# Optimization experiments

Measured on AMD Instinct MI355X. Metric: run time of the kernel, lower is better.

## Reference

```python
import jax, jax.numpy as jnp
import numpy as np

S, HID, H, KH, D = 2048, 3584, 28, 4, 128
G = H // KH  # GQA group size = 7
EPS = 1e-6
THETA = 1000000.0


def _rmsnorm(x, w, eps=EPS):
    v = jnp.mean(x.astype(jnp.float32) ** 2, axis=-1, keepdims=True)
    return (x * jax.lax.rsqrt(v + eps)).astype(x.dtype) * w


def setup_inputs() -> dict:
    key = jax.random.key(0)
    k1, k2, k3, k4 = jax.random.split(key, 4)
    return {
        "positions": jnp.arange(S, dtype=jnp.int32),
        "hidden_states": jax.random.normal(k1, (S, HID), dtype=jnp.float32),
        "qkv_w": jax.random.normal(k2, ((H + 2 * KH) * D, HID), dtype=jnp.float32) * (1.0 / np.sqrt(HID)),
        "qkv_b": jax.random.normal(k3, ((H + 2 * KH) * D,), dtype=jnp.float32) * 0.02,
        "q_norm_w": jnp.ones((H * D,), dtype=jnp.float32),
        "k_norm_w": jnp.ones((KH * D,), dtype=jnp.float32),
        "o_w": jax.random.normal(k4, (HID, H * D), dtype=jnp.float32) * (1.0 / np.sqrt(H * D)),
    }


def reference(positions, hidden_states, qkv_w, qkv_b, q_norm_w, k_norm_w, o_w):
    # QKV projection (fused linear, bias=True)
    qkv = hidden_states @ qkv_w.T + qkv_b  # [S, (H+2*KH)*D]
    q, k, v = jnp.split(qkv, [H * D, H * D + KH * D], axis=-1)

    # olmo-style QK RMSNorm over the full (all-heads-concatenated) q/k vectors
    q = _rmsnorm(q, q_norm_w)
    k = _rmsnorm(k, k_norm_w)

    # NeoX-style RoPE (vLLM default): rotate halves
    half = D // 2
    inv_freq = 1.0 / (THETA ** (jnp.arange(0, D, 2, dtype=jnp.float32) / D))  # [D/2]
    freqs = positions[:, None].astype(jnp.float32) * inv_freq  # [S, D/2]
    cos = jnp.cos(freqs)[:, None, :]  # [S, 1, D/2]
    sin = jnp.sin(freqs)[:, None, :]

    def rope(x, nh):
        x = x.reshape(S, nh, D)
        x1, x2 = x[..., :half], x[..., half:]
        return jnp.concatenate([x1 * cos - x2 * sin, x2 * cos + x1 * sin], axis=-1)

    q = rope(q, H)            # [S, H, D]
    k = rope(k, KH)           # [S, KH, D]
    v = v.reshape(S, KH, D)   # [S, KH, D]

    # Grouped-query causal attention
    qg = q.reshape(S, KH, G, D)
    scores = jnp.einsum('skgd,tkd->kgst', qg, k) * (D ** -0.5)  # [KH, G, S, S]
    causal = positions[:, None] >= positions[None, :]  # [S, S]
    scores = jnp.where(causal[None, None], scores, jnp.finfo(scores.dtype).min)
    probs = jax.nn.softmax(scores, axis=-1)
    attn = jnp.einsum('kgst,tkd->skgd', probs, v).reshape(S, H * D)

    # Output projection (bias=False)
    return attn @ o_w.T  # [S, HID]
```

## Files before the change

### kernel.cpp

```cpp
#include <hip/hip_runtime.h>
#include <hip/hip_bf16.h>
#include <stdint.h>

#define S_LEN 2048
#define HIDDEN 3584
#define NH 28
#define NKH 4
#define DH 128
#define NG 7
#define NQKV 4608
#define QD 3584
#define KD 512

using bf16x8 = __attribute__((ext_vector_type(8))) __bf16;
using f32x4  = __attribute__((ext_vector_type(4))) float;
using f32x16 = __attribute__((ext_vector_type(16))) float;

#define AS3(p) ((__attribute__((address_space(3))) void*)(p))
#define AS1(p) ((const __attribute__((address_space(1))) void*)(p))

__device__ __forceinline__ unsigned short f2bf(float f) {
    unsigned u = __float_as_uint(f);
    u += 0x7FFFu + ((u >> 16) & 1u);
    return (unsigned short)(u >> 16);
}
__device__ __forceinline__ unsigned cvtpk(float a, float b) {
    unsigned r;
    asm("v_cvt_pk_bf16_f32 %0, %1, %2" : "=v"(r) : "v"(a), "v"(b));
    return r;
}

__global__ void cvt2_f32_bf16(const float* __restrict__ a, unsigned short* __restrict__ oa, int na4,
                              const float* __restrict__ b, unsigned short* __restrict__ ob, int nb4) {
    int i = blockIdx.x * blockDim.x + threadIdx.x;
    const float* src;
    unsigned short* dst;
    int n;
    if (i < na4)            { src = a; dst = oa; n = i; }
    else if (i < na4 + nb4) { src = b; dst = ob; n = i - na4; }
    else return;
    float4 v = ((const float4*)src)[n];
    ushort4 o;
    o.x = f2bf(v.x); o.y = f2bf(v.y); o.z = f2bf(v.z); o.w = f2bf(v.w);
    ((ushort4*)dst)[n] = o;
}

__global__ void cvt_f32_bf16(const float* __restrict__ in,
                             unsigned short* __restrict__ out, int n4) {
    int i = blockIdx.x * blockDim.x + threadIdx.x;
    if (i >= n4) return;
    float4 v = ((const float4*)in)[i];
    ushort4 o;
    o.x = f2bf(v.x); o.y = f2bf(v.y); o.z = f2bf(v.z); o.w = f2bf(v.w);
    ((ushort4*)out)[i] = o;
}

template<int BN>
__global__ __launch_bounds__(512, 2) void gemm_deep(
    const unsigned short* __restrict__ A,
    const unsigned short* __restrict__ B,
    float* __restrict__ C,
    const float* __restrict__ bias,
    int M, int N, int K)
{
    constexpr int NF    = BN / 64;
    constexpr int WN    = BN / 4;
    constexpr int VB    = BN / 64;
    constexpr int TILEB = (256 + BN) * 128;
    __shared__ __align__(16) unsigned char ds[2 * TILEB];

    const int tid  = threadIdx.x;
    const int w    = tid >> 6;
    const int lane = tid & 63;
    const int lr   = lane & 15;
    const int lg   = lane >> 4;
    const int wr   = w >> 2;
    const int wc   = w & 3;
    const int m0   = blockIdx.y * 256;
    const int n0   = blockIdx.x * BN;
    const long K2  = (long)K * 2;
    const int scw  = 16 * ((tid & 7) ^ ((tid >> 3) & 7));
    const int srow = tid >> 3;
    const unsigned char* Ab = (const unsigned char*)A;
    const unsigned char* Bb = (const unsigned char*)B;
    const int nk = K >> 6;

    unsigned char* buf0 = ds;
    unsigned char* buf1 = ds + TILEB;

    auto stageB = [&](int kt, unsigned char* bufp) {
        const long kb = (long)kt * 128;
        #pragma unroll
        for (int k = 0; k < VB; ++k)
            __builtin_amdgcn_global_load_lds(
                AS1(Bb + (long)(n0 + k * 64 + srow) * K2 + kb + scw),
                AS3(bufp + k * 8192 + w * 1024), 16, 0, 0);
    };
    auto stageA = [&](int kt, unsigned char* bufp) {
        const long kb = (long)kt * 128;
        #pragma unroll
        for (int k = 0; k < 4; ++k)
            __builtin_amdgcn_global_load_lds(
                AS1(Ab + (long)(m0 + k * 64 + srow) * K2 + kb + scw),
                AS3(bufp + VB * 8192 + k * 8192 + w * 1024), 16, 0, 0);
    };

    f32x4  acc[8][NF] = {};
    bf16x8 af[4][2], bf[NF][2];

    auto readA = [&](const unsigned char* bufp, int half) {
        #pragma unroll
        for (int i = 0; i < 4; ++i) {
            const int row = wr * 128 + (half * 4 + i) * 16 + lr;
            #pragma unroll
            for (int kk = 0; kk < 2; ++kk)
                af[i][kk] = *(const bf16x8*)(bufp + VB * 8192 + row * 128 +
                                             ((kk * 64 + lg * 16) ^ ((lr & 7) << 4)));
        }
    };
    auto readB = [&](const unsigned char* bufp) {
        #pragma unroll
        for (int ni = 0; ni < NF; ++ni) {
            const int row = wc * WN + ni * 16 + lr;
            #pragma unroll
            for (int kk = 0; kk < 2; ++kk)
                bf[ni][kk] = *(const bf16x8*)(bufp + row * 128 +
                                              ((kk * 64 + lg * 16) ^ ((lr & 7) << 4)));
        }
    };
    auto mfmah = [&](int half) {
        __builtin_amdgcn_s_setprio(1);
        #pragma unroll
        for (int i = 0; i < 4; ++i)
            #pragma unroll
            for (int ni = 0; ni < NF; ++ni)
                #pragma unroll
                for (int kk = 0; kk < 2; ++kk)
                    acc[half * 4 + i][ni] = __builtin_amdgcn_mfma_f32_16x16x32_bf16(
                        af[i][kk], bf[ni][kk], acc[half * 4 + i][ni], 0, 0, 0);
        __builtin_amdgcn_s_setprio(0);
    };

    #define VMC() do { if constexpr (VB == 3) asm volatile("s_waitcnt vmcnt(3)" ::: "memory"); \
                       else                   asm volatile("s_waitcnt vmcnt(2)" ::: "memory"); } while (0)
    #define LGK0() do { asm volatile("s_waitcnt lgkmcnt(0)" ::: "memory"); \
                        __builtin_amdgcn_sched_barrier(0); } while (0)

    stageB(0, buf0); stageA(0, buf0); stageB(1, buf1);
    VMC();
    __builtin_amdgcn_s_barrier();

    const int npairs = nk >> 1;
    for (int p = 0; p < npairs; ++p) {
        const int to = 2 * p + 1;
        int te2 = 2 * p + 2; if (te2 >= nk) te2 = nk - 1;
        int to2 = 2 * p + 3; if (to2 >= nk) to2 = nk - 1;

        readA(buf0, 0); readB(buf0);
        stageA(to, buf1);
        __builtin_amdgcn_s_barrier();
        LGK0();
        mfmah(0);
        __builtin_amdgcn_s_barrier();
        readA(buf0, 1);
        stageB(te2, buf0);
        __builtin_amdgcn_s_barrier();
        LGK0();
        mfmah(1);
        VMC();
        __builtin_amdgcn_s_barrier();
        readA(buf1, 0); readB(buf1);
        stageA(te2, buf0);
        __builtin_amdgcn_s_barrier();
        LGK0();
        mfmah(0);
        __builtin_amdgcn_s_barrier();
        readA(buf1, 1);
        stageB(to2, buf1);
        __builtin_amdgcn_s_barrier();
        LGK0();
        mfmah(1);
        VMC();
        __builtin_amdgcn_s_barrier();
    }
    asm volatile("s_waitcnt vmcnt(0)" ::: "memory");

    #pragma unroll
    for (int mi = 0; mi < 8; ++mi) {
        #pragma unroll
        for (int ni = 0; ni < NF; ++ni) {
            const int col = n0 + wc * WN + ni * 16 + lr;
            const float bv = bias ? bias[col] : 0.0f;
            #pragma unroll
            for (int j = 0; j < 4; ++j) {
                const int row = m0 + wr * 128 + mi * 16 + lg * 4 + j;
                C[(long)row * N + col] = acc[mi][ni][j] + bv;
            }
        }
    }
    #undef VMC
    #undef LGK0
}

__global__ __launch_bounds__(256) void qkv_post(
    const float* __restrict__ qkv,
    const int* __restrict__ positions,
    const float* __restrict__ qnw,
    const float* __restrict__ knw,
    unsigned short* __restrict__ qb,
    unsigned short* __restrict__ kb,
    unsigned short* __restrict__ vt2)
{
    const int s   = blockIdx.x;
    const int tid = threadIdx.x;
    const float* rowp = qkv + (long)s * NQKV;
    __shared__ float red[256];
    __shared__ float s_rq, s_rk;

    float aq = 0.f;
    for (int i = tid; i < QD; i += 256) { float v = rowp[i]; aq += v * v; }
    red[tid] = aq; __syncthreads();
    for (int off = 128; off > 0; off >>= 1) {
        if (tid < off) red[tid] += red[tid + off];
        __syncthreads();
    }
    if (tid == 0) s_rq = rsqrtf(red[0] / (float)QD + 1e-6f);
    __syncthreads();

    float ak = 0.f;
    for (int i = tid; i < KD; i += 256) { float v = rowp[QD + i]; ak += v * v; }
    red[tid] = ak; __syncthreads();
    for (int off = 128; off > 0; off >>= 1) {
        if (tid < off) red[tid] += red[tid + off];
        __syncthreads();
    }
    if (tid == 0) s_rk = rsqrtf(red[0] / (float)KD + 1e-6f);
    __syncthreads();

    const float rq  = s_rq, rk = s_rk * 0.08838834764831845f;
    const float pos = (float)positions[s];
    const float c_lnf = 0.21586735253866598f;

    for (int u = tid; u < NH * 64; u += 256) {
        const int h = u >> 6, j = u & 63;
        const float inv = expf(-(float)j * c_lnf);
        float sn, cs;
        sincosf(pos * inv, &sn, &cs);
        const float x1 = rowp[h * DH + j]      * rq * qnw[h * DH + j];
        const float x2 = rowp[h * DH + 64 + j] * rq * qnw[h * DH + 64 + j];
        qb[((long)h * S_LEN + s) * DH + j]      = f2bf(x1 * cs - x2 * sn);
        qb[((long)h * S_LEN + s) * DH + 64 + j] = f2bf(x2 * cs + x1 * sn);
    }
    for (int u = tid; u < NKH * 64; u += 256) {
        const int h = u >> 6, j = u & 63;
        const float inv = expf(-(float)j * c_lnf);
        float sn, cs;
        sincosf(pos * inv, &sn, &cs);
        const float x1 = rowp[QD + h * DH + j]      * rk * knw[h * DH + j];
        const float x2 = rowp[QD + h * DH + 64 + j] * rk * knw[h * DH + 64 + j];
        kb[((long)h * S_LEN + s) * DH + j]      = f2bf(x1 * cs - x2 * sn);
        kb[((long)h * S_LEN + s) * DH + 64 + j] = f2bf(x2 * cs + x1 * sn);
    }
    for (int u = tid; u < KD; u += 256) {
        const int hh = u >> 7, d = u & 127;
        vt2[(((long)hh * (S_LEN / 32) + (s >> 5)) * DH + d) * 32 + (s & 31)] =
            f2bf(rowp[QD + KD + u]);
    }
}

__global__ __launch_bounds__(512) void attn_fwd(
    const unsigned short* __restrict__ qb,
    const unsigned short* __restrict__ kb,
    const unsigned short* __restrict__ vt2,
    unsigned short* __restrict__ attnb)
{
    __shared__ __align__(16) unsigned char sK[2][8192];
    __shared__ __align__(16) unsigned char sV[2][8192];

    const int qt   = 63 - blockIdx.x;
    const int kh   = blockIdx.y;
    const int tid  = threadIdx.x;
    const int w    = tid >> 6;
    const int lane = tid & 63;
    const int lq   = lane & 31;
    const int hi   = lane >> 5;
    const int hi8  = hi * 8;
    const int hi4  = hi * 4;
    const int q0   = qt * 32;
    const int NT   = qt + 1;

    const unsigned char* kgb = (const unsigned char*)(kb + (long)kh * S_LEN * DH);
    const unsigned char* vgb = (const unsigned char*)vt2 + (long)kh * (S_LEN / 32) * 8192;

    const int ksrc_off = (((tid & 15) ^ (tid >> 4)) & 15) << 4;
    const int u        = tid & 255;
    const int vsrc_off = ((u & 3) ^ ((u >> 3) & 3)) << 4;

    const float RTHR = 8.0f;

    bf16x8 qf[8];
    if (w < 7) {
        const int h = kh * NG + w;
        const unsigned short* qrow = qb + ((long)h * S_LEN + q0 + lq) * DH;
        #pragma unroll
        for (int c = 0; c < 8; ++c)
            qf[c] = *(const bf16x8*)(qrow + c * 16 + hi8);
    }

    f32x16 o[4] = {};
    float m = -3e38f;
    float l = 0.f;

    if (tid < 256) {
        #pragma unroll
        for (int j = 0; j < 2; ++j)
            __builtin_amdgcn_global_load_lds(AS1(kgb + ((tid >> 4) + 16 * j) * 256 + ksrc_off),
                                             AS3(&sK[0][0] + w * 1024 + j * 4096), 16, 0, 0);
    } else {
        #pragma unroll
        for (int j = 0; j < 2; ++j)
            __builtin_amdgcn_global_load_lds(AS1(vgb + ((u >> 2) + 64 * j) * 64 + vsrc_off),
                                             AS3(&sV[0][0] + (w - 4) * 1024 + j * 4096), 16, 0, 0);
    }

    for (int t = 0; t < NT; ++t) {
        __syncthreads();

        if (t + 1 < NT) {
            const int b = (t + 1) & 1;
            if (tid < 256) {
                const unsigned char* ks = kgb + (long)(t + 1) * 8192;
                #pragma unroll
                for (int j = 0; j < 2; ++j)
                    __builtin_amdgcn_global_load_lds(AS1(ks + ((tid >> 4) + 16 * j) * 256 + ksrc_off),
                                                     AS3(&sK[b][0] + w * 1024 + j * 4096), 16, 0, 0);
            } else {
                const unsigned char* vs = vgb + (long)(t + 1) * 8192;
                #pragma unroll
                for (int j = 0; j < 2; ++j)
                    __builtin_amdgcn_global_load_lds(AS1(vs + ((u >> 2) + 64 * j) * 64 + vsrc_off),
                                                     AS3(&sV[b][0] + (w - 4) * 1024 + j * 4096), 16, 0, 0);
            }
        }

        if (w < 7) {
            const unsigned char* sKb = sK[t & 1];
            const unsigned char* sVb = sV[t & 1];

            bf16x8 kf[8];
            #pragma unroll
            for (int c = 0; c < 8; ++c)
                kf[c] = *(const bf16x8*)(sKb + lq * 256 + (((2 * c + hi) ^ (lq & 15)) << 4));
            f32x16 sc = {};
            #pragma unroll
            for (int c = 0; c < 8; ++c)
                sc = __builtin_amdgcn_mfma_f32_32x32x16_bf16(kf[c], qf[c], sc, 0, 0, 0);

            float s[16];
            if (t == NT - 1) {
                #pragma unroll
                for (int r = 0; r < 16; ++r) {
                    const int kr = (r & 3) + 8 * (r >> 2) + hi4;
                    s[r] = (kr > lq) ? -3e38f : sc[r];
                }
            } else {
                #pragma unroll
                for (int r = 0; r < 16; ++r) s[r] = sc[r];
            }

            float mx = s[0];
            #pragma unroll
            for (int r = 1; r < 16; ++r) mx = fmaxf(mx, s[r]);
            mx = fmaxf(mx, __shfl_xor(mx, 32));

            if (!__all(mx <= m + RTHR)) {
                const float nm  = fmaxf(m, mx);
                const float fac = __expf(m - nm);
                l *= fac;
                #pragma unroll
                for (int d0 = 0; d0 < 4; ++d0)
                    #pragma unroll
                    for (int r = 0; r < 16; ++r) o[d0][r] *= fac;
                m = nm;
            }

            float p[16];
            float ps = 0.f;
            #pragma unroll
            for (int r = 0; r < 16; ++r) {
                p[r] = __expf(s[r] - m);
                ps += p[r];
            }
            ps += __shfl_xor(ps, 32);
            l += ps;

            unsigned pa01 = cvtpk(p[0],  p[1]),  pa23 = cvtpk(p[2],  p[3]);
            unsigned pb01 = cvtpk(p[4],  p[5]),  pb23 = cvtpk(p[6],  p[7]);
            unsigned pc01 = cvtpk(p[8],  p[9]),  pc23 = cvtpk(p[10], p[11]);
            unsigned pd01 = cvtpk(p[12], p[13]), pd23 = cvtpk(p[14], p[15]);
            unsigned xa01 = __shfl_xor((int)pa01, 32), xa23 = __shfl_xor((int)pa23, 32);
            unsigned xb01 = __shfl_xor((int)pb01, 32), xb23 = __shfl_xor((int)pb23, 32);
            unsigned xc01 = __shfl_xor((int)pc01, 32), xc23 = __shfl_xor((int)pc23, 32);
            unsigned xd01 = __shfl_xor((int)pd01, 32), xd23 = __shfl_xor((int)pd23, 32);

            union { unsigned uu[4]; bf16x8 v; } pf0, pf1;
            pf0.uu[0] = hi ? xb01 : pa01;
            pf0.uu[1] = hi ? xb23 : pa23;
            pf0.uu[2] = hi ? pb01 : xa01;
            pf0.uu[3] = hi ? pb23 : xa23;
            pf1.uu[0] = hi ? xd01 : pc01;
            pf1.uu[1] = hi ? xd23 : pc23;
            pf1.uu[2] = hi ? pd01 : xc01;
            pf1.uu[3] = hi ? pd23 : xc23;

            #pragma unroll
            for (int d0 = 0; d0 < 4; ++d0) {
                const int row = d0 * 32 + lq;
                const int sw  = (lq >> 1) & 3;
                bf16x8 vf0 = *(const bf16x8*)(sVb + row * 64 + ((hi ^ sw) << 4));
                bf16x8 vf1 = *(const bf16x8*)(sVb + row * 64 + (((2 + hi) ^ sw) << 4));
                o[d0] = __builtin_amdgcn_mfma_f32_32x32x16_bf16(vf0, pf0.v, o[d0], 0, 0, 0);
                o[d0] = __builtin_amdgcn_mfma_f32_32x32x16_bf16(vf1, pf1.v, o[d0], 0, 0, 0);
            }
        }
    }

    if (w == 7) return;

    const float rl = 1.0f / l;
    unsigned short* orow = attnb + (long)(q0 + lq) * QD + (kh * NG + w) * DH;
    #pragma unroll
    for (int d0 = 0; d0 < 4; ++d0) {
        #pragma unroll
        for (int g = 0; g < 4; ++g) {
            ushort4 s4;
            s4.x = f2bf(o[d0][4 * g + 0] * rl);
            s4.y = f2bf(o[d0][4 * g + 1] * rl);
            s4.z = f2bf(o[d0][4 * g + 2] * rl);
            s4.w = f2bf(o[d0][4 * g + 3] * rl);
            *(ushort4*)(orow + d0 * 32 + 8 * g + hi4) = s4;
        }
    }
}

extern "C" void kernel_launch(void* const* d_in, const int* in_sizes, int n_in,
                              void* d_out, int out_size, void* d_ws, size_t ws_size,
                              hipStream_t stream) {
    const int*   positions = (const int*)d_in[0];
    const float* hidden    = (const float*)d_in[1];
    const float* qkv_w     = (const float*)d_in[2];
    const float* qkv_b     = (const float*)d_in[3];
    const float* qnw       = (const float*)d_in[4];
    const float* knw       = (const float*)d_in[5];
    const float* o_w       = (const float*)d_in[6];
    float* out = (float*)d_out;

    unsigned char* ws = (unsigned char*)d_ws;
    unsigned short* hb    = (unsigned short*)(ws);
    unsigned short* w1    = (unsigned short*)(ws + 14680064);
    float*          qkvf  = (float*)(ws + 47710208);
    unsigned short* qbuf  = (unsigned short*)(ws + 85458944);
    unsigned short* kbuf  = (unsigned short*)(ws + 100139008);
    unsigned short* vtb   = (unsigned short*)(ws + 102236160);
    unsigned short* attnb = (unsigned short*)(ws);
    unsigned short* w2    = (unsigned short*)(ws + 14680064);

    const int na4 = S_LEN * HIDDEN / 4;
    const int nb4 = NQKV * HIDDEN / 4;
    cvt2_f32_bf16<<<(na4 + nb4 + 255) / 256, 256, 0, stream>>>(hidden, hb, na4, qkv_w, w1, nb4);
    gemm_deep<192><<<dim3(NQKV / 192, S_LEN / 256), 512, 0, stream>>>(
        hb, w1, qkvf, qkv_b, S_LEN, NQKV, HIDDEN);
    qkv_post<<<S_LEN, 256, 0, stream>>>(qkvf, positions, qnw, knw, qbuf, kbuf, vtb);
    attn_fwd<<<dim3(S_LEN / 32, NKH), 512, 0, stream>>>(qbuf, kbuf, vtb, attnb);
    cvt_f32_bf16<<<(HIDDEN * QD / 4 + 255) / 256, 256, 0, stream>>>(o_w, w2, HIDDEN * QD / 4);
    gemm_deep<128><<<dim3(HIDDEN / 128, S_LEN / 256), 512, 0, stream>>>(
        attnb, w2, out, nullptr, S_LEN, HIDDEN, QD);
}
```

Baseline: 261.7 us.

## Split causal attention KV loop across two blocks with a combine pass

The attention kernel now runs with a third grid dimension of 2. Each block handles every other KV tile, so the grid doubles and the longest causal query tiles get roughly half the serial work. Each split writes unnormalized fp32 partial outputs plus per-row max and sum to workspace. A new combine kernel merges the two splits with log-sum-exp rescaling and writes the bf16 attention output. The cost is a large fp32 partial-output write and read-back, plus an extra kernel launch.

```diff
diff --git a/kernel.cpp b/kernel.cpp
--- a/kernel.cpp
+++ b/kernel.cpp
@@ -268,17 +268,19 @@
     }
 }
 
-__global__ __launch_bounds__(512) void attn_fwd(
+__global__ __launch_bounds__(512) void attn_split(
     const unsigned short* __restrict__ qb,
     const unsigned short* __restrict__ kb,
     const unsigned short* __restrict__ vt2,
-    unsigned short* __restrict__ attnb)
+    float* __restrict__ pO,
+    float* __restrict__ pml)
 {
     __shared__ __align__(16) unsigned char sK[2][8192];
     __shared__ __align__(16) unsigned char sV[2][8192];
 
     const int qt   = 63 - blockIdx.x;
     const int kh   = blockIdx.y;
+    const int z    = blockIdx.z;
     const int tid  = threadIdx.x;
     const int w    = tid >> 6;
     const int lane = tid & 63;
@@ -298,6 +300,22 @@
 
     const float RTHR = 8.0f;
 
+    auto stage = [&](int t, int b) {
+        if (tid < 256) {
+            const unsigned char* ks = kgb + (long)t * 8192;
+            #pragma unroll
+            for (int j = 0; j < 2; ++j)
+                __builtin_amdgcn_global_load_lds(AS1(ks + ((tid >> 4) + 16 * j) * 256 + ksrc_off),
+                                                 AS3(&sK[b][0] + w * 1024 + j * 4096), 16, 0, 0);
+        } else {
+            const unsigned char* vs = vgb + (long)t * 8192;
+            #pragma unroll
+            for (int j = 0; j < 2; ++j)
+                __builtin_amdgcn_global_load_lds(AS1(vs + ((u >> 2) + 64 * j) * 64 + vsrc_off),
+                                                 AS3(&sV[b][0] + (w - 4) * 1024 + j * 4096), 16, 0, 0);
+        }
+    };
+
     bf16x8 qf[8];
     if (w < 7) {
         const int h = kh * NG + w;
@@ -311,41 +329,17 @@
     float m = -3e38f;
     float l = 0.f;
 
-    if (tid < 256) {
-        #pragma unroll
-        for (int j = 0; j < 2; ++j)
-            __builtin_amdgcn_global_load_lds(AS1(kgb + ((tid >> 4) + 16 * j) * 256 + ksrc_off),
-                                             AS3(&sK[0][0] + w * 1024 + j * 4096), 16, 0, 0);
-    } else {
-        #pragma unroll
-        for (int j = 0; j < 2; ++j)
-            __builtin_amdgcn_global_load_lds(AS1(vgb + ((u >> 2) + 64 * j) * 64 + vsrc_off),
-                                             AS3(&sV[0][0] + (w - 4) * 1024 + j * 4096), 16, 0, 0);
-    }
-
-    for (int t = 0; t < NT; ++t) {
+    stage(z, 0);
+
+    int ii = 0;
+    for (int t = z; t < NT; t += 2, ++ii) {
         __syncthreads();
 
-        if (t + 1 < NT) {
-            const int b = (t + 1) & 1;
-            if (tid < 256) {
-                const unsigned char* ks = kgb + (long)(t + 1) * 8192;
-                #pragma unroll
-                for (int j = 0; j < 2; ++j)
-                    __builtin_amdgcn_global_load_lds(AS1(ks + ((tid >> 4) + 16 * j) * 256 + ksrc_off),
-                                                     AS3(&sK[b][0] + w * 1024 + j * 4096), 16, 0, 0);
-            } else {
-                const unsigned char* vs = vgb + (long)(t + 1) * 8192;
-                #pragma unroll
-                for (int j = 0; j < 2; ++j)
-                    __builtin_amdgcn_global_load_lds(AS1(vs + ((u >> 2) + 64 * j) * 64 + vsrc_off),
-                                                     AS3(&sV[b][0] + (w - 4) * 1024 + j * 4096), 16, 0, 0);
-            }
-        }
+        if (t + 2 < NT) stage(t + 2, (ii + 1) & 1);
 
         if (w < 7) {
-            const unsigned char* sKb = sK[t & 1];
-            const unsigned char* sVb = sV[t & 1];
+            const unsigned char* sKb = sK[ii & 1];
+            const unsigned char* sVb = sV[ii & 1];
 
             bf16x8 kf[8];
             #pragma unroll
@@ -427,19 +421,61 @@
 
     if (w == 7) return;
 
-    const float rl = 1.0f / l;
-    unsigned short* orow = attnb + (long)(q0 + lq) * QD + (kh * NG + w) * DH;
+    const long rec = ((long)(z * NKH + kh) * 64 + qt) * 7 + w;
+    float* Orec = pO + rec * 4096;
     #pragma unroll
     for (int d0 = 0; d0 < 4; ++d0) {
         #pragma unroll
         for (int g = 0; g < 4; ++g) {
-            ushort4 s4;
-            s4.x = f2bf(o[d0][4 * g + 0] * rl);
-            s4.y = f2bf(o[d0][4 * g + 1] * rl);
-            s4.z = f2bf(o[d0][4 * g + 2] * rl);
-            s4.w = f2bf(o[d0][4 * g + 3] * rl);
-            *(ushort4*)(orow + d0 * 32 + 8 * g + hi4) = s4;
+            float4 s4;
+            s4.x = o[d0][4 * g + 0];
+            s4.y = o[d0][4 * g + 1];
+            s4.z = o[d0][4 * g + 2];
+            s4.w = o[d0][4 * g + 3];
+            *(float4*)(Orec + lq * 128 + d0 * 32 + 8 * g + hi4) = s4;
         }
+    }
+    if (hi == 0) {
+        pml[rec * 64 + lq]      = m;
+        pml[rec * 64 + 32 + lq] = l;
+    }
+}
+
+__global__ __launch_bounds__(256) void attn_combine(
+    const float* __restrict__ pO,
+    const float* __restrict__ pml,
+    unsigned short* __restrict__ attnb)
+{
+    const int qt  = blockIdx.x;
+    const int h   = blockIdx.y;
+    const int kh  = h / NG;
+    const int wh  = h % NG;
+    const int tid = threadIdx.x;
+    const int q   = tid >> 3;
+    const int dg  = (tid & 7) * 16;
+
+    const long rec0 = ((long)kh * 64 + qt) * 7 + wh;
+    const long rec1 = rec0 + (long)NKH * 64 * 7;
+    const float m0 = pml[rec0 * 64 + q], l0 = pml[rec0 * 64 + 32 + q];
+    const float m1 = pml[rec1 * 64 + q], l1 = pml[rec1 * 64 + 32 + q];
+    const float M  = fmaxf(m0, m1);
+    const float f0 = __expf(m0 - M);
+    const float f1 = __expf(m1 - M);
+    const float rl = 1.0f / (l0 * f0 + l1 * f1);
+
+    const float* O0 = pO + rec0 * 4096 + q * 128 + dg;
+    const float* O1 = pO + rec1 * 4096 + q * 128 + dg;
+    unsigned short* orow = attnb + (long)(qt * 32 + q) * QD + h * DH + dg;
+    #pragma unroll
+    for (int i = 0; i < 4; ++i) {
+        float4 a = *(const float4*)(O0 + i * 4);
+        float4 b = *(const float4*)(O1 + i * 4);
+        ushort4 s4;
+        s4.x = f2bf((f0 * a.x + f1 * b.x) * rl);
+        s4.y = f2bf((f0 * a.y + f1 * b.y) * rl);
+        s4.z = f2bf((f0 * a.z + f1 * b.z) * rl);
+        s4.w = f2bf((f0 * a.w + f1 * b.w) * rl);
+        *(ushort4*)(orow + i * 4) = s4;
     }
 }
 
@@ -463,6 +499,8 @@
     unsigned short* kbuf  = (unsigned short*)(ws + 100139008);
     unsigned short* vtb   = (unsigned short*)(ws + 102236160);
     unsigned short* attnb = (unsigned short*)(ws);
+    float*          pO    = (float*)(ws + 14680064);
+    float*          pml   = (float*)(ws + 73400320);
     unsigned short* w2    = (unsigned short*)(ws + 14680064);
 
     const int na4 = S_LEN * HIDDEN / 4;
@@ -471,7 +509,8 @@
     gemm_deep<192><<<dim3(NQKV / 192, S_LEN / 256), 512, 0, stream>>>(
         hb, w1, qkvf, qkv_b, S_LEN, NQKV, HIDDEN);
     qkv_post<<<S_LEN, 256, 0, stream>>>(qkvf, positions, qnw, knw, qbuf, kbuf, vtb);
-    attn_fwd<<<dim3(S_LEN / 32, NKH), 512, 0, stream>>>(qbuf, kbuf, vtb, attnb);
+    attn_split<<<dim3(S_LEN / 32, NKH, 2), 512, 0, stream>>>(qbuf, kbuf, vtb, pO, pml);
+    attn_combine<<<dim3(S_LEN / 32, NH), 256, 0, stream>>>(pO, pml, attnb);
     cvt_f32_bf16<<<(HIDDEN * QD / 4 + 255) / 256, 256, 0, stream>>>(o_w, w2, HIDDEN * QD / 4);
     gemm_deep<128><<<dim3(HIDDEN / 128, S_LEN / 256), 512, 0, stream>>>(
         attnb, w2, out, nullptr, S_LEN, HIDDEN, QD);
```

Result: slower. 276.3 us (+5.6%).
